# Kernel tuning notes

Measured on AMD Instinct MI355X. Metric: run time of the kernel, lower is better.

The kernel has to match this reference:

```python
import jax, jax.numpy as jnp
import numpy as np

L, B, H, C, Y = 128, 256, 256, 17, 16   # seq len, batch, hidden, control channels (u_size+1), obs dim
N_SUB = 2                               # euler substeps per knot interval


def setup_inputs() -> dict:
    key = jax.random.key(0)
    ks = jax.random.split(key, 8)
    t = jnp.arange(L, dtype=jnp.float32) * 0.1
    ts = jnp.broadcast_to(t[:, None, None], (L, B, 1))
    us = jax.random.normal(ks[0], (L, B, C - 1), dtype=jnp.float32)
    ys = jax.random.normal(ks[1], (L, B, Y), dtype=jnp.float32)
    s1 = 1.0 / np.sqrt(C)
    s2 = 1.0 / np.sqrt(H)
    return {
        "ts": ts, "us": us, "ys": ys, "batch_size": B,
        "enc_W": jax.random.normal(ks[2], (C, H), dtype=jnp.float32) * s1,
        "enc_b": jnp.zeros((H,), jnp.float32),
        "dec_W": jax.random.normal(ks[3], (H, Y), dtype=jnp.float32) * s2,
        "dec_b": jnp.zeros((Y,), jnp.float32),
        "f_W1": jax.random.normal(ks[4], (H, H), dtype=jnp.float32) * s2,
        "f_b1": jnp.zeros((H,), jnp.float32),
        "f_W2": jax.random.normal(ks[5], (H, H * C), dtype=jnp.float32) * s2,
        "f_b2": jnp.zeros((H * C,), jnp.float32),
    }


def _hermite_coeffs(t, x):
    # torchcde hermite_cubic_coefficients_with_backward_differences:
    # knot derivatives m[i] = (x_i - x_{i-1}) / (t_i - t_{i-1}), m[0] = m[1]
    dt = t[1:] - t[:-1]                       # (l-1,)
    h = dt[None, :, None]
    slope = (x[:, 1:] - x[:, :-1]) / h        # (b, l-1, c)
    m = jnp.concatenate([slope[:, :1], slope], axis=1)
    mi, mn = m[:, :-1], m[:, 1:]
    xi, xn = x[:, :-1], x[:, 1:]
    c2 = 3.0 * (xn - xi) / h**2 - (2.0 * mi + mn) / h
    c3 = 2.0 * (xi - xn) / h**3 + (mi + mn) / h**2
    return mi, c2, c3, dt


def _forward(ts, us, enc_W, enc_b, dec_W, dec_b, f_W1, f_b1, f_W2, f_b2):
    t = ts[:, 0, 0]                                            # (l,)
    x = jnp.concatenate([ts, us], axis=-1).transpose(1, 0, 2)  # (b, l, c)
    mi, c2, c3, dt = _hermite_coeffs(t, x)
    b = x.shape[0]
    z0 = jnp.zeros((b, C), x.dtype) @ enc_W + enc_b            # encoder(zeros)

    def f(z):  # NCDE vector field: (b,h) -> (b,h,c)
        hdn = jax.nn.relu(z @ f_W1 + f_b1)
        return jnp.tanh(hdn @ f_W2 + f_b2).reshape(b, H, C)

    def step(z, args):
        m_, c2_, c3_, h_ = args                                # (b,c)x3, scalar
        for j in range(N_SUB):  # fixed small unroll, not a data-dim loop
            u = h_ * (j / N_SUB)
            dX = m_ + 2.0 * c2_ * u + 3.0 * c3_ * u * u        # spline derivative, (b,c)
            z = z + jnp.einsum('bhc,bc->bh', f(z), dX) * (h_ / N_SUB)
        return z, z

    _, zs = jax.lax.scan(
        step, z0,
        (mi.transpose(1, 0, 2), c2.transpose(1, 0, 2), c3.transpose(1, 0, 2), dt))
    zs = jnp.concatenate([z0[None], zs], axis=0)               # (l, b, h)
    return zs @ dec_W + dec_b                                  # (l, b, y)


def reference(ts, us, ys, batch_size, enc_W, enc_b, dec_W, dec_b, f_W1, f_b1, f_W2, f_b2):
    return _forward(ts, us, enc_W, enc_b, dec_W, dec_b, f_W1, f_b1, f_W2, f_b2)
```

## Files before the change

kernel.cpp:

```cpp
#include <hip/hip_runtime.h>
#include <hip/hip_bf16.h>
#include <cmath>

#define L_   128
#define B_   256
#define H_   256
#define C_   17
#define Y_   16
#define NSUB 254
#define NGRP 16
#define RNK  16

typedef short bf16x8 __attribute__((ext_vector_type(8)));
typedef float f32x4  __attribute__((ext_vector_type(4)));
typedef unsigned short u16;
typedef unsigned int   u32;

#define OFF_DXR  0u
#define OFF_W2H  5201920u
#define OFF_W2L  7823360u
#define OFF_W1H  10444800u
#define OFF_W1L  10575872u
#define OFF_DEH  10706944u
#define OFF_DEL  10715136u
#define OFF_ZFH  10723328u
#define OFF_ZFL  10985472u
#define OFF_ZM   11247616u

__device__ __forceinline__ float fast_tanh(float x) {
  float e = __expf(2.0f * x);
  return 1.0f - __fdividef(2.0f, e + 1.0f);
}

__device__ __forceinline__ void bsplit(float x, u16& hi, u16& lo) {
  __hip_bfloat16 h = __float2bfloat16(x);
  float hf = __bfloat162float(h);
  __hip_bfloat16 l = __float2bfloat16(x - hf);
  hi = *(u16*)&h;
  lo = *(u16*)&l;
}

__global__ void k_dx(const float* __restrict__ ts, const float* __restrict__ us,
                     float* __restrict__ dXr) {
  int idx = blockIdx.x * 256 + threadIdx.x;
  int c   = idx % 20;
  int t2  = idx / 20;
  int b   = t2 & 255;
  int sub = t2 >> 8;
  if (c >= C_) { dXr[idx] = 0.f; return; }
  int s = sub >> 1, j = sub & 1;
  float t_s = ts[s * B_], t_n = ts[(s + 1) * B_];
  float h = t_n - t_s;
  float xi, xn;
  if (c == 0) { xi = ts[s * B_ + b]; xn = ts[(s + 1) * B_ + b]; }
  else {
    xi = us[(size_t)s       * 4096 + b * 16 + (c - 1)];
    xn = us[(size_t)(s + 1) * 4096 + b * 16 + (c - 1)];
  }
  float mn = (xn - xi) / h;
  float mi;
  if (s == 0) mi = mn;
  else {
    float hp = t_s - ts[(s - 1) * B_];
    float xp = (c == 0) ? ts[(s - 1) * B_ + b]
                        : us[(size_t)(s - 1) * 4096 + b * 16 + (c - 1)];
    mi = (xi - xp) / hp;
  }
  float c2 = 3.f * (xn - xi) / (h * h) - (2.f * mi + mn) / h;
  float c3 = 2.f * (xi - xn) / (h * h * h) + (mi + mn) / (h * h);
  float u  = j ? 0.5f * h : 0.f;
  float dX = mi + 2.f * c2 * u + 3.f * c3 * u * u;
  dXr[idx] = dX * 0.5f * h;
}

__global__ void k_w2f(const float* __restrict__ W2,
                      u16* __restrict__ WH, u16* __restrict__ WL) {
  int idx = blockIdx.x * 256 + threadIdx.x;
  int e = idx & 7, lane = (idx >> 3) & 63, kt = (idx >> 9) & 7;
  int t = idx >> 12;
  int mt = t % 20, r = t / 20;
  int col = mt * 16 + (lane & 15);
  int hl = col / 20, c = col - hl * 20;
  int k = kt * 32 + 4 * (lane >> 4) + (e & 3) + 16 * (e >> 2);
  float v = (c < C_) ? W2[(size_t)k * (H_ * C_) + (r * 16 + hl) * C_ + c] : 0.f;
  u16 hi, lo; bsplit(v, hi, lo);
  WH[idx] = hi; WL[idx] = lo;
}

__global__ void k_w1f(const float* __restrict__ W1,
                      u16* __restrict__ WH, u16* __restrict__ WL) {
  int idx = blockIdx.x * 256 + threadIdx.x;
  int e = idx & 7, lane = (idx >> 3) & 63, kt = (idx >> 9) & 7, mtg = idx >> 12;
  int m = mtg * 16 + (lane & 15);
  int k = kt * 32 + 4 * (lane >> 4) + (e & 3) + 16 * (e >> 2);
  float v = W1[k * 256 + m];
  u16 hi, lo; bsplit(v, hi, lo);
  WH[idx] = hi; WL[idx] = lo;
}

__global__ void k_def(const float* __restrict__ decW,
                      u16* __restrict__ DH, u16* __restrict__ DL) {
  int idx = blockIdx.x * 256 + threadIdx.x;
  int e = idx & 7, lane = (idx >> 3) & 63, kt = idx >> 9;
  int y = lane & 15;
  int k = kt * 32 + 4 * (lane >> 4) + (e & 3) + 16 * (e >> 2);
  float v = decW[k * 16 + y];
  u16 hi, lo; bsplit(v, hi, lo);
  DH[idx] = hi; DL[idx] = lo;
}

__global__ void k_initF(const float* __restrict__ enc_b,
                        u16* __restrict__ ZH, u16* __restrict__ ZL) {
  int idx = blockIdx.x * 256 + threadIdx.x;
  int e = idx & 7, lane = (idx >> 3) & 63;
  int kt = (idx >> 9) & 7;
  int h = kt * 32 + 4 * (lane >> 4) + (e & 3) + 16 * (e >> 2);
  float v = enc_b[h];
  u16 hi, lo; bsplit(v, hi, lo);
  ZH[idx] = hi; ZL[idx] = lo;
}

__global__ void k_zm0(const float* __restrict__ enc_b, float* __restrict__ zM) {
  int idx = blockIdx.x * 256 + threadIdx.x;
  zM[idx] = enc_b[(idx >> 4) & 255];
}

__global__ __launch_bounds__(256, 1)
void k_step(char* __restrict__ wsb, const float* __restrict__ f_b1,
            const float* __restrict__ f_b2, const float* __restrict__ dec_b,
            float* __restrict__ out, int sub) {
  const int tid = threadIdx.x, lane = tid & 63, kq = tid >> 6;
  const int grp = blockIdx.x >> 4, rank = blockIdx.x & 15;
  const int gg = lane >> 4, c16 = lane & 15;

  if (sub == NSUB && rank != 0) return;

  __shared__ __align__(16) char smem[38400];
  u16* zsH = (u16*)smem;
  u16* zsL = (u16*)(smem + 8192);
  u16* hxH = (u16*)(smem + 16384);
  u16* hxL = (u16*)(smem + 24576);
  f32x4* red4 = (f32x4*)(smem + 32768);
  float* b1L  = (float*)(smem + 35840);
  float* b2L  = (float*)(smem + 36864);

  b1L[tid] = f_b1[tid];
  for (int i = tid; i < 320; i += 256) {
    int hl = i / 20, c = i - hl * 20;
    b2L[i] = (c < C_) ? f_b2[(rank * 16 + hl) * C_ + c] : 0.f;
  }

  const bf16x8* W2Hg = (const bf16x8*)(wsb + OFF_W2H);
  const bf16x8* W2Lg = (const bf16x8*)(wsb + OFF_W2L);
  const bf16x8* W1Hg = (const bf16x8*)(wsb + OFF_W1H);
  const bf16x8* W1Lg = (const bf16x8*)(wsb + OFF_W1L);
  const bf16x8* DHg  = (const bf16x8*)(wsb + OFF_DEH);
  const bf16x8* DLg  = (const bf16x8*)(wsb + OFF_DEL);
  const float*  dXr  = (const float*)(wsb + OFF_DXR);
  float* zM = (float*)(wsb + OFF_ZM) + ((size_t)(grp * 16 + rank)) * 256;

  float zm[4];
  #pragma unroll
  for (int hh = 0; hh < 4; ++hh)
    zm[hh] = zM[(4 * kq + hh) * 16 + c16];

  {
    const f32x4* gzH = (const f32x4*)(wsb + OFF_ZFH +
                         ((size_t)(sub & 1) * NGRP + grp) * 8192);
    const f32x4* gzL = (const f32x4*)(wsb + OFF_ZFL +
                         ((size_t)(sub & 1) * NGRP + grp) * 8192);
    ((f32x4*)zsH)[tid]       = gzH[tid];
    ((f32x4*)zsH)[tid + 256] = gzH[tid + 256];
    ((f32x4*)zsL)[tid]       = gzL[tid];
    ((f32x4*)zsL)[tid + 256] = gzL[tid + 256];
  }
  __syncthreads();

  if (((sub & 1) == 0) && rank == 0) {
    f32x4 ad = (f32x4){0.f, 0.f, 0.f, 0.f};
    #pragma unroll
    for (int ktl = 0; ktl < 2; ++ktl) {
      int kt = kq * 2 + ktl;
      bf16x8 dh = DHg[kt * 64 + lane], dl = DLg[kt * 64 + lane];
      bf16x8 zh = ((const bf16x8*)zsH)[kt * 64 + lane];
      bf16x8 zl = ((const bf16x8*)zsL)[kt * 64 + lane];
      ad = __builtin_amdgcn_mfma_f32_16x16x32_bf16(dh, zh, ad, 0, 0, 0);
      ad = __builtin_amdgcn_mfma_f32_16x16x32_bf16(dh, zl, ad, 0, 0, 0);
      ad = __builtin_amdgcn_mfma_f32_16x16x32_bf16(dl, zh, ad, 0, 0, 0);
    }
    if (kq) red4[(kq - 1) * 64 + lane] = ad;
    __syncthreads();
    if (kq == 0) {
      #pragma unroll
      for (int q = 0; q < 3; ++q) ad += red4[q * 64 + lane];
      float4 q0;
      q0.x = ad[0] + dec_b[4 * gg + 0]; q0.y = ad[1] + dec_b[4 * gg + 1];
      q0.z = ad[2] + dec_b[4 * gg + 2]; q0.w = ad[3] + dec_b[4 * gg + 3];
      *(float4*)(out + (size_t)(sub >> 1) * 4096 +
                 (grp * 16 + c16) * 16 + 4 * gg) = q0;
    }
    __syncthreads();
  }
  if (sub == NSUB) return;

  f32x4 aa[4];
  #pragma unroll
  for (int mm = 0; mm < 4; ++mm) aa[mm] = (f32x4){0.f, 0.f, 0.f, 0.f};
  #pragma unroll
  for (int kt = 0; kt < 8; ++kt) {
    bf16x8 zh = ((const bf16x8*)zsH)[kt * 64 + lane];
    bf16x8 zl = ((const bf16x8*)zsL)[kt * 64 + lane];
    #pragma unroll
    for (int mm = 0; mm < 4; ++mm) {
      bf16x8 wh = W1Hg[((4 * kq + mm) * 8 + kt) * 64 + lane];
      bf16x8 wl = W1Lg[((4 * kq + mm) * 8 + kt) * 64 + lane];
      aa[mm] = __builtin_amdgcn_mfma_f32_16x16x32_bf16(wh, zh, aa[mm], 0, 0, 0);
      aa[mm] = __builtin_amdgcn_mfma_f32_16x16x32_bf16(wh, zl, aa[mm], 0, 0, 0);
      aa[mm] = __builtin_amdgcn_mfma_f32_16x16x32_bf16(wl, zh, aa[mm], 0, 0, 0);
    }
  }

  {
    bf16x8 hH[2], hL[2];
    #pragma unroll
    for (int mm = 0; mm < 4; ++mm)
      #pragma unroll
      for (int r = 0; r < 4; ++r) {
        float v = aa[mm][r] + b1L[kq * 64 + mm * 16 + 4 * gg + r];
        v = fmaxf(v, 0.f);
        u16 hi, lo; bsplit(v, hi, lo);
        hH[mm >> 1][r + 4 * (mm & 1)] = (short)hi;
        hL[mm >> 1][r + 4 * (mm & 1)] = (short)lo;
      }
    ((bf16x8*)hxH)[(2 * kq + 0) * 64 + lane] = hH[0];
    ((bf16x8*)hxH)[(2 * kq + 1) * 64 + lane] = hH[1];
    ((bf16x8*)hxL)[(2 * kq + 0) * 64 + lane] = hL[0];
    ((bf16x8*)hxL)[(2 * kq + 1) * 64 + lane] = hL[1];
  }
  __syncthreads();

  f32x4 ab[5];
  #pragma unroll
  for (int ml = 0; ml < 5; ++ml) ab[ml] = (f32x4){0.f, 0.f, 0.f, 0.f};
  #pragma unroll
  for (int kt = 0; kt < 8; ++kt) {
    bf16x8 hh = ((const bf16x8*)hxH)[kt * 64 + lane];
    bf16x8 hl = ((const bf16x8*)hxL)[kt * 64 + lane];
    #pragma unroll
    for (int ml = 0; ml < 5; ++ml) {
      bf16x8 wh = W2Hg[(((rank * 20 + kq * 5 + ml) * 8) + kt) * 64 + lane];
      bf16x8 wl = W2Lg[(((rank * 20 + kq * 5 + ml) * 8) + kt) * 64 + lane];
      ab[ml] = __builtin_amdgcn_mfma_f32_16x16x32_bf16(wh, hh, ab[ml], 0, 0, 0);
      ab[ml] = __builtin_amdgcn_mfma_f32_16x16x32_bf16(wh, hl, ab[ml], 0, 0, 0);
      ab[ml] = __builtin_amdgcn_mfma_f32_16x16x32_bf16(wl, hh, ab[ml], 0, 0, 0);
    }
  }

  {
    float ph[4] = {0.f, 0.f, 0.f, 0.f};
    #pragma unroll
    for (int ml = 0; ml < 5; ++ml) {
      int col0 = (kq * 5 + ml) * 16 + 4 * gg;
      int hl_  = col0 / 20;
      int c0   = col0 - hl_ * 20;
      float4 b2v = *(const float4*)&b2L[col0];
      float4 dxv = *(const float4*)(dXr +
          ((size_t)sub * 256 + grp * 16 + c16) * 20 + c0);
      float t0 = fast_tanh(ab[ml][0] + b2v.x);
      float t1 = fast_tanh(ab[ml][1] + b2v.y);
      float t2 = fast_tanh(ab[ml][2] + b2v.z);
      float t3 = fast_tanh(ab[ml][3] + b2v.w);
      float contrib = fmaf(t0, dxv.x, fmaf(t1, dxv.y, fmaf(t2, dxv.z, t3 * dxv.w)));
      int hrel = hl_ - 4 * kq;
      #pragma unroll
      for (int hh = 0; hh < 4; ++hh)
        ph[hh] += (hrel == hh) ? contrib : 0.f;
    }
    #pragma unroll
    for (int hh = 0; hh < 4; ++hh) {
      float v = ph[hh];
      v += __shfl_xor(v, 16);
      v += __shfl_xor(v, 32);
      zm[hh] += v;
    }
    if (gg == 0) {
      #pragma unroll
      for (int hh = 0; hh < 4; ++hh)
        zM[(4 * kq + hh) * 16 + c16] = zm[hh];
      int hg0 = rank * 16 + 4 * kq;
      int ktf = hg0 >> 5, kl0 = hg0 & 31;
      int lp  = c16 + 16 * ((kl0 >> 2) & 3);
      int e0  = 4 * ((kl0 >> 4) & 1);
      int fi  = (ktf * 64 + lp) * 8 + e0;
      u16* zdH = (u16*)(wsb + OFF_ZFH) +
                 ((size_t)((sub + 1) & 1) * NGRP + grp) * 4096;
      u16* zdL = (u16*)(wsb + OFF_ZFL) +
                 ((size_t)((sub + 1) & 1) * NGRP + grp) * 4096;
      ushort4 vh, vl;
      u16 h0, l0;
      bsplit(zm[0], h0, l0); vh.x = h0; vl.x = l0;
      bsplit(zm[1], h0, l0); vh.y = h0; vl.y = l0;
      bsplit(zm[2], h0, l0); vh.z = h0; vl.z = l0;
      bsplit(zm[3], h0, l0); vh.w = h0; vl.w = l0;
      *(ushort4*)(zdH + fi) = vh;
      *(ushort4*)(zdL + fi) = vl;
    }
  }
}

extern "C" void kernel_launch(void* const* d_in, const int* in_sizes, int n_in,
                              void* d_out, int out_size, void* d_ws, size_t ws_size,
                              hipStream_t stream) {
  const float* ts    = (const float*)d_in[0];
  const float* us    = (const float*)d_in[1];
  const float* enc_b = (const float*)d_in[5];
  const float* dec_W = (const float*)d_in[6];
  const float* dec_b = (const float*)d_in[7];
  const float* f_W1  = (const float*)d_in[8];
  const float* f_b1  = (const float*)d_in[9];
  const float* f_W2  = (const float*)d_in[10];
  const float* f_b2  = (const float*)d_in[11];
  float* out = (float*)d_out;
  char* wsb = (char*)d_ws;

  k_dx   <<<5080, 256, 0, stream>>>(ts, us, (float*)(wsb + OFF_DXR));
  k_w2f  <<<5120, 256, 0, stream>>>(f_W2, (u16*)(wsb + OFF_W2H), (u16*)(wsb + OFF_W2L));
  k_w1f  <<<256, 256, 0, stream>>>(f_W1, (u16*)(wsb + OFF_W1H), (u16*)(wsb + OFF_W1L));
  k_def  <<<16, 256, 0, stream>>>(dec_W, (u16*)(wsb + OFF_DEH), (u16*)(wsb + OFF_DEL));
  k_initF<<<256, 256, 0, stream>>>(enc_b, (u16*)(wsb + OFF_ZFH), (u16*)(wsb + OFF_ZFL));
  k_zm0  <<<256, 256, 0, stream>>>(enc_b, (float*)(wsb + OFF_ZM));

  for (int sub = 0; sub <= NSUB; ++sub)
    k_step<<<256, 256, 0, stream>>>(wsb, f_b1, f_b2, dec_b, out, sub);
}
```

Measured before the change: 2.941 ms.

## Split per-block work across eight waves instead of four in step kernel

Doubles the step kernel's block size to 512 threads. Each wave now handles half as many W1 output tiles and about three W2 tiles instead of five, so per-wave MFMA chains are shorter and more waves per CU can hide global-load latency of the weights. The tanh/dX reduction now skips tiles that do not belong to the wave's two hidden rows, and the write-back packs two values instead of four. The cost is adjacent waves overlapping on one W2 tile (computed twice), a larger shared-memory allocation, and an eight-way reduction in the decoder path.

```diff
diff --git a/kernel.cpp b/kernel.cpp
--- a/kernel.cpp
+++ b/kernel.cpp
@@ -125,27 +125,27 @@
   zM[idx] = enc_b[(idx >> 4) & 255];
 }
 
-__global__ __launch_bounds__(256, 1)
+__global__ __launch_bounds__(512, 1)
 void k_step(char* __restrict__ wsb, const float* __restrict__ f_b1,
             const float* __restrict__ f_b2, const float* __restrict__ dec_b,
             float* __restrict__ out, int sub) {
-  const int tid = threadIdx.x, lane = tid & 63, kq = tid >> 6;
+  const int tid = threadIdx.x, lane = tid & 63, wq = tid >> 6;
   const int grp = blockIdx.x >> 4, rank = blockIdx.x & 15;
   const int gg = lane >> 4, c16 = lane & 15;
 
   if (sub == NSUB && rank != 0) return;
 
-  __shared__ __align__(16) char smem[38400];
+  __shared__ __align__(16) char smem[84096];
   u16* zsH = (u16*)smem;
   u16* zsL = (u16*)(smem + 8192);
   u16* hxH = (u16*)(smem + 16384);
   u16* hxL = (u16*)(smem + 24576);
   f32x4* red4 = (f32x4*)(smem + 32768);
-  float* b1L  = (float*)(smem + 35840);
-  float* b2L  = (float*)(smem + 36864);
-
-  b1L[tid] = f_b1[tid];
-  for (int i = tid; i < 320; i += 256) {
+  float* b1L  = (float*)(smem + 40960);
+  float* b2L  = (float*)(smem + 41984);
+
+  if (tid < 256) b1L[tid] = f_b1[tid];
+  for (int i = tid; i < 320; i += 512) {
     int hl = i / 20, c = i - hl * 20;
     b2L[i] = (c < C_) ? f_b2[(rank * 16 + hl) * C_ + c] : 0.f;
   }
@@ -159,40 +159,35 @@
   const float*  dXr  = (const float*)(wsb + OFF_DXR);
   float* zM = (float*)(wsb + OFF_ZM) + ((size_t)(grp * 16 + rank)) * 256;
 
-  float zm[4];
-  #pragma unroll
-  for (int hh = 0; hh < 4; ++hh)
-    zm[hh] = zM[(4 * kq + hh) * 16 + c16];
+  float zm[2];
+  zm[0] = zM[(2 * wq + 0) * 16 + c16];
+  zm[1] = zM[(2 * wq + 1) * 16 + c16];
 
   {
     const f32x4* gzH = (const f32x4*)(wsb + OFF_ZFH +
                          ((size_t)(sub & 1) * NGRP + grp) * 8192);
     const f32x4* gzL = (const f32x4*)(wsb + OFF_ZFL +
                          ((size_t)(sub & 1) * NGRP + grp) * 8192);
-    ((f32x4*)zsH)[tid]       = gzH[tid];
-    ((f32x4*)zsH)[tid + 256] = gzH[tid + 256];
-    ((f32x4*)zsL)[tid]       = gzL[tid];
-    ((f32x4*)zsL)[tid + 256] = gzL[tid + 256];
+    ((f32x4*)zsH)[tid] = gzH[tid];
+    ((f32x4*)zsL)[tid] = gzL[tid];
   }
   __syncthreads();
 
   if (((sub & 1) == 0) && rank == 0) {
     f32x4 ad = (f32x4){0.f, 0.f, 0.f, 0.f};
-    #pragma unroll
-    for (int ktl = 0; ktl < 2; ++ktl) {
-      int kt = kq * 2 + ktl;
-      bf16x8 dh = DHg[kt * 64 + lane], dl = DLg[kt * 64 + lane];
-      bf16x8 zh = ((const bf16x8*)zsH)[kt * 64 + lane];
-      bf16x8 zl = ((const bf16x8*)zsL)[kt * 64 + lane];
+    {
+      bf16x8 dh = DHg[wq * 64 + lane], dl = DLg[wq * 64 + lane];
+      bf16x8 zh = ((const bf16x8*)zsH)[wq * 64 + lane];
+      bf16x8 zl = ((const bf16x8*)zsL)[wq * 64 + lane];
       ad = __builtin_amdgcn_mfma_f32_16x16x32_bf16(dh, zh, ad, 0, 0, 0);
       ad = __builtin_amdgcn_mfma_f32_16x16x32_bf16(dh, zl, ad, 0, 0, 0);
       ad = __builtin_amdgcn_mfma_f32_16x16x32_bf16(dl, zh, ad, 0, 0, 0);
     }
-    if (kq) red4[(kq - 1) * 64 + lane] = ad;
+    if (wq) red4[(wq - 1) * 64 + lane] = ad;
     __syncthreads();
-    if (kq == 0) {
+    if (wq == 0) {
       #pragma unroll
-      for (int q = 0; q < 3; ++q) ad += red4[q * 64 + lane];
+      for (int q = 0; q < 7; ++q) ad += red4[q * 64 + lane];
       float4 q0;
       q0.x = ad[0] + dec_b[4 * gg + 0]; q0.y = ad[1] + dec_b[4 * gg + 1];
       q0.z = ad[2] + dec_b[4 * gg + 2]; q0.w = ad[3] + dec_b[4 * gg + 3];
@@ -203,17 +198,18 @@
   }
   if (sub == NSUB) return;
 
-  f32x4 aa[4];
-  #pragma unroll
-  for (int mm = 0; mm < 4; ++mm) aa[mm] = (f32x4){0.f, 0.f, 0.f, 0.f};
+  f32x4 aa[2];
+  aa[0] = (f32x4){0.f, 0.f, 0.f, 0.f};
+  aa[1] = (f32x4){0.f, 0.f, 0.f, 0.f};
   #pragma unroll
   for (int kt = 0; kt < 8; ++kt) {
     bf16x8 zh = ((const bf16x8*)zsH)[kt * 64 + lane];
     bf16x8 zl = ((const bf16x8*)zsL)[kt * 64 + lane];
     #pragma unroll
-    for (int mm = 0; mm < 4; ++mm) {
-      bf16x8 wh = W1Hg[((4 * kq + mm) * 8 + kt) * 64 + lane];
-      bf16x8 wl = W1Lg[((4 * kq + mm) * 8 + kt) * 64 + lane];
+    for (int mm = 0; mm < 2; ++mm) {
+      int mtg = 2 * wq + mm;
+      bf16x8 wh = W1Hg[(mtg * 8 + kt) * 64 + lane];
+      bf16x8 wl = W1Lg[(mtg * 8 + kt) * 64 + lane];
       aa[mm] = __builtin_amdgcn_mfma_f32_16x16x32_bf16(wh, zh, aa[mm], 0, 0, 0);
       aa[mm] = __builtin_amdgcn_mfma_f32_16x16x32_bf16(wh, zl, aa[mm], 0, 0, 0);
       aa[mm] = __builtin_amdgcn_mfma_f32_16x16x32_bf16(wl, zh, aa[mm], 0, 0, 0);
@@ -221,35 +217,34 @@
   }
 
   {
-    bf16x8 hH[2], hL[2];
-    #pragma unroll
-    for (int mm = 0; mm < 4; ++mm)
+    bf16x8 hH, hL;
+    #pragma unroll
+    for (int mm = 0; mm < 2; ++mm)
       #pragma unroll
       for (int r = 0; r < 4; ++r) {
-        float v = aa[mm][r] + b1L[kq * 64 + mm * 16 + 4 * gg + r];
+        float v = aa[mm][r] + b1L[(2 * wq + mm) * 16 + 4 * gg + r];
         v = fmaxf(v, 0.f);
         u16 hi, lo; bsplit(v, hi, lo);
-        hH[mm >> 1][r + 4 * (mm & 1)] = (short)hi;
-        hL[mm >> 1][r + 4 * (mm & 1)] = (short)lo;
+        hH[r + 4 * mm] = (short)hi;
+        hL[r + 4 * mm] = (short)lo;
       }
-    ((bf16x8*)hxH)[(2 * kq + 0) * 64 + lane] = hH[0];
-    ((bf16x8*)hxH)[(2 * kq + 1) * 64 + lane] = hH[1];
-    ((bf16x8*)hxL)[(2 * kq + 0) * 64 + lane] = hL[0];
-    ((bf16x8*)hxL)[(2 * kq + 1) * 64 + lane] = hL[1];
+    ((bf16x8*)hxH)[wq * 64 + lane] = hH;
+    ((bf16x8*)hxL)[wq * 64 + lane] = hL;
   }
   __syncthreads();
 
-  f32x4 ab[5];
+  const int m0 = (5 * wq) >> 1;
+  f32x4 ab[3];
   #pragma unroll
-  for (int ml = 0; ml < 5; ++ml) ab[ml] = (f32x4){0.f, 0.f, 0.f, 0.f};
+  for (int ml = 0; ml < 3; ++ml) ab[ml] = (f32x4){0.f, 0.f, 0.f, 0.f};
   #pragma unroll
   for (int kt = 0; kt < 8; ++kt) {
     bf16x8 hh = ((const bf16x8*)hxH)[kt * 64 + lane];
     bf16x8 hl = ((const bf16x8*)hxL)[kt * 64 + lane];
     #pragma unroll
-    for (int ml = 0; ml < 5; ++ml) {
-      bf16x8 wh = W2Hg[(((rank * 20 + kq * 5 + ml) * 8) + kt) * 64 + lane];
-      bf16x8 wl = W2Lg[(((rank * 20 + kq * 5 + ml) * 8) + kt) * 64 + lane];
+    for (int ml = 0; ml < 3; ++ml) {
+      bf16x8 wh = W2Hg[(((rank * 20 + m0 + ml) * 8) + kt) * 64 + lane];
+      bf16x8 wl = W2Lg[(((rank * 20 + m0 + ml) * 8) + kt) * 64 + lane];
       ab[ml] = __builtin_amdgcn_mfma_f32_16x16x32_bf16(wh, hh, ab[ml], 0, 0, 0);
       ab[ml] = __builtin_amdgcn_mfma_f32_16x16x32_bf16(wh, hl, ab[ml], 0, 0, 0);
       ab[ml] = __builtin_amdgcn_mfma_f32_16x16x32_bf16(wl, hh, ab[ml], 0, 0, 0);
@@ -257,53 +252,48 @@
   }
 
   {
-    float ph[4] = {0.f, 0.f, 0.f, 0.f};
-    #pragma unroll
-    for (int ml = 0; ml < 5; ++ml) {
-      int col0 = (kq * 5 + ml) * 16 + 4 * gg;
+    float ph[2] = {0.f, 0.f};
+    #pragma unroll
+    for (int ml = 0; ml < 3; ++ml) {
+      int col0 = (m0 + ml) * 16 + 4 * gg;
       int hl_  = col0 / 20;
-      int c0   = col0 - hl_ * 20;
-      float4 b2v = *(const float4*)&b2L[col0];
-      float4 dxv = *(const float4*)(dXr +
-          ((size_t)sub * 256 + grp * 16 + c16) * 20 + c0);
-      float t0 = fast_tanh(ab[ml][0] + b2v.x);
-      float t1 = fast_tanh(ab[ml][1] + b2v.y);
-      float t2 = fast_tanh(ab[ml][2] + b2v.z);
-      float t3 = fast_tanh(ab[ml][3] + b2v.w);
-      float contrib = fmaf(t0, dxv.x, fmaf(t1, dxv.y, fmaf(t2, dxv.z, t3 * dxv.w)));
-      int hrel = hl_ - 4 * kq;
-      #pragma unroll
-      for (int hh = 0; hh < 4; ++hh)
-        ph[hh] += (hrel == hh) ? contrib : 0.f;
-    }
-    #pragma unroll
-    for (int hh = 0; hh < 4; ++hh) {
+      if ((hl_ >> 1) == wq) {
+        int c0 = col0 - hl_ * 20;
+        float4 b2v = *(const float4*)&b2L[col0];
+        float4 dxv = *(const float4*)(dXr +
+            ((size_t)sub * 256 + grp * 16 + c16) * 20 + c0);
+        float t0 = fast_tanh(ab[ml][0] + b2v.x);
+        float t1 = fast_tanh(ab[ml][1] + b2v.y);
+        float t2 = fast_tanh(ab[ml][2] + b2v.z);
+        float t3 = fast_tanh(ab[ml][3] + b2v.w);
+        float contrib = fmaf(t0, dxv.x, fmaf(t1, dxv.y, fmaf(t2, dxv.z, t3 * dxv.w)));
+        ph[hl_ & 1] += contrib;
+      }
+    }
+    #pragma unroll
+    for (int hh = 0; hh < 2; ++hh) {
       float v = ph[hh];
       v += __shfl_xor(v, 16);
       v += __shfl_xor(v, 32);
       zm[hh] += v;
     }
     if (gg == 0) {
-      #pragma unroll
-      for (int hh = 0; hh < 4; ++hh)
-        zM[(4 * kq + hh) * 16 + c16] = zm[hh];
-      int hg0 = rank * 16 + 4 * kq;
-      int ktf = hg0 >> 5, kl0 = hg0 & 31;
-      int lp  = c16 + 16 * ((kl0 >> 2) & 3);
-      int e0  = 4 * ((kl0 >> 4) & 1);
+      zM[(2 * wq + 0) * 16 + c16] = zm[0];
+      zM[(2 * wq + 1) * 16 + c16] = zm[1];
+      int ktf = rank >> 1;
+      int lp  = c16 + 16 * (wq >> 1);
+      int e0  = ((2 * wq) & 3) + 4 * (rank & 1);
       int fi  = (ktf * 64 + lp) * 8 + e0;
       u16* zdH = (u16*)(wsb + OFF_ZFH) +
                  ((size_t)((sub + 1) & 1) * NGRP + grp) * 4096;
       u16* zdL = (u16*)(wsb + OFF_ZFL) +
                  ((size_t)((sub + 1) & 1) * NGRP + grp) * 4096;
-      ushort4 vh, vl;
+      ushort2 vh, vl;
       u16 h0, l0;
       bsplit(zm[0], h0, l0); vh.x = h0; vl.x = l0;
       bsplit(zm[1], h0, l0); vh.y = h0; vl.y = l0;
-      bsplit(zm[2], h0, l0); vh.z = h0; vl.z = l0;
-      bsplit(zm[3], h0, l0); vh.w = h0; vl.w = l0;
-      *(ushort4*)(zdH + fi) = vh;
-      *(ushort4*)(zdL + fi) = vl;
+      *(ushort2*)(zdH + fi) = vh;
+      *(ushort2*)(zdL + fi) = vl;
     }
   }
 }
@@ -331,5 +321,5 @@
   k_zm0  <<<256, 256, 0, stream>>>(enc_b, (float*)(wsb + OFF_ZM));
 
   for (int sub = 0; sub <= NSUB; ++sub)
-    k_step<<<256, 256, 0, stream>>>(wsb, f_b1, f_b2, dec_b, out, sub);
-}
+    k_step<<<256, 512, 0, stream>>>(wsb, f_b1, f_b2, dec_b, out, sub);
+}
```

Measured after the change: 2.517 ms. 1.17x faster.
